# Kernel optimization log

Hardware: AMD Instinct MI355X
Metric: run time of the kernel (lower is better)

## Reference

```python
import jax, jax.numpy as jnp
import numpy as np

B, L, DIN, DOUT, H, N, NLAYERS, NRES, NSPECIES = 32, 2048, 5, 5, 256, 32, 4, 3, 100


def conv1d(x, w, b, pad):
    # x: (B, Cin, L), w: (Cout, Cin, K)
    y = jax.lax.conv_general_dilated(x, w, (1,), [(pad, pad)], dimension_numbers=('NCH', 'OIH', 'NCH'))
    return y + b[None, :, None]


def layer_norm_c(x, g, b):
    # LayerNorm over channel dim of (B, H, L) (matches norm(x.transpose(-1,-2)).transpose(-1,-2))
    mu = x.mean(1, keepdims=True)
    v = ((x - mu) ** 2).mean(1, keepdims=True)
    return (x - mu) / jnp.sqrt(v + 1e-5) * g[None, :, None] + b[None, :, None]


def dss_layer(x, log_dt, lam_re, lam_im, W_re, W_im, D, glu_w, glu_b):
    # Bidirectional diagonal state-space (DSS) layer, transposed layout (B, H, L).
    Bb, Hh, Ll = x.shape
    dt = jnp.exp(log_dt)                                  # (H,)
    lam = lam_re + 1j * lam_im                            # (N,) with Re(lam) < 0
    pos = jnp.arange(Ll)
    # Vandermonde: E[h,n,l] = exp(dt[h] * lam[n] * l)
    E = jnp.exp(dt[:, None, None] * lam[None, :, None] * pos[None, None, :])  # (H,N,L) complex
    W = W_re + 1j * W_im                                  # (2,H,N) fwd/bwd kernels
    k = jnp.einsum('chn,hnl->chl', W, E).real             # (2,H,L)
    zpad = jnp.zeros_like(k[0])
    k2 = jnp.concatenate([k[0], zpad], -1) + jnp.concatenate([zpad, k[1][:, ::-1]], -1)  # (H,2L)
    # FFT circular conv of length 2L -> linear conv, keep first L
    y = jnp.fft.irfft(jnp.fft.rfft(x, 2 * Ll) * jnp.fft.rfft(k2, 2 * Ll)[None], 2 * Ll)[..., :Ll]
    y = y + D[None, :, None] * x
    y = jax.nn.gelu(y, approximate=False)
    # postact GLU via position-wise linear H -> 2H
    z = jnp.einsum('oh,bhl->bol', glu_w, y) + glu_b[None, :, None]
    return z[:, :Hh] * jax.nn.sigmoid(z[:, Hh:])


def setup_inputs():
    key = jax.random.key(0)
    ks = jax.random.split(key, 20)
    g = lambda i, shape, s=0.05: jax.random.normal(ks[i], shape, jnp.float32) * s
    inp = {}
    inp['x'] = jax.random.normal(ks[0], (B, DIN, L), jnp.float32)
    inp['xs'] = jax.random.randint(ks[1], (B,), 0, NSPECIES)
    inp['enc_w'] = g(2, (H, DIN, 15))
    inp['enc_b'] = jnp.zeros((H,), jnp.float32)
    inp['res_w1'] = g(3, (NRES, H, H, 3), 0.02)
    inp['res_b1'] = jnp.zeros((NRES, H), jnp.float32)
    inp['res_w2'] = g(4, (NRES, H, H, 3), 0.02)
    inp['res_b2'] = jnp.zeros((NRES, H), jnp.float32)
    inp['log_dt'] = jax.random.uniform(ks[5], (NLAYERS, H), jnp.float32, float(np.log(1e-3)), float(np.log(1e-1)))
    inp['lam_re'] = -(0.1 + jax.random.uniform(ks[6], (NLAYERS, N), jnp.float32))
    inp['lam_im'] = jnp.broadcast_to(jnp.pi * jnp.arange(N, dtype=jnp.float32), (NLAYERS, N)) + 0.0
    inp['W_re'] = g(7, (NLAYERS, 2, H, N), 0.1)
    inp['W_im'] = g(8, (NLAYERS, 2, H, N), 0.1)
    inp['D'] = g(9, (NLAYERS, H), 1.0)
    inp['glu_w'] = g(10, (NLAYERS, 2 * H, H))
    inp['glu_b'] = jnp.zeros((NLAYERS, 2 * H), jnp.float32)
    inp['ln_g'] = jnp.ones((NLAYERS, H), jnp.float32)
    inp['ln_b'] = jnp.zeros((NLAYERS, H), jnp.float32)
    inp['dec_w'] = g(11, (DOUT, H, 15))
    inp['dec_b'] = jnp.zeros((DOUT,), jnp.float32)
    inp['sp_emb'] = g(12, (NSPECIES, H), 0.02)
    inp['h1_w'] = g(13, (128, 256)); inp['h1_b'] = jnp.zeros((128,), jnp.float32)
    inp['h2_w'] = g(14, (64, 128)); inp['h2_b'] = jnp.zeros((64,), jnp.float32)
    inp['h3_w'] = g(15, (32, 64)); inp['h3_b'] = jnp.zeros((32,), jnp.float32)
    inp['h4_w'] = g(16, (1, 32)); inp['h4_b'] = jnp.zeros((1,), jnp.float32)
    return inp


def _forward(x, xs, enc_w, enc_b, res_w1, res_b1, res_w2, res_b2, log_dt, lam_re, lam_im, W_re, W_im, D, glu_w, glu_b, ln_g, ln_b, dec_w, dec_b, sp_emb, h1_w, h1_b, h2_w, h2_b, h3_w, h3_b, h4_w, h4_b):
    h = conv1d(x, enc_w, enc_b, 7)
    for i in range(NRES):  # L1Block resnet stack (dropout/BN are identity at eval)
        r = jax.nn.relu(conv1d(h, res_w1[i], res_b1[i], 1))
        r = conv1d(r, res_w2[i], res_b2[i], 1)
        h = jax.nn.relu(r + h)
    for i in range(NLAYERS):  # post-norm DSS blocks
        z = dss_layer(h, log_dt[i], lam_re[i], lam_im[i], W_re[i], W_im[i], D[i], glu_w[i], glu_b[i])
        h = layer_norm_c(z + h, ln_g[i], ln_b[i])
    h = h + sp_emb[xs][:, :, None]  # species encoder (embed_before=False)
    seq_emb = h
    agg = h.mean(-1)  # (B, H)
    r = jax.nn.elu(agg @ h1_w.T + h1_b)
    r = jax.nn.elu(r @ h2_w.T + h2_b)
    r = jax.nn.elu(r @ h3_w.T + h3_b)
    reg_y = r @ h4_w.T + h4_b
    dec = conv1d(h, dec_w, dec_b, 7)
    return dec, seq_emb, reg_y


def reference(x, xs, enc_w, enc_b, res_w1, res_b1, res_w2, res_b2, log_dt, lam_re, lam_im, W_re, W_im, D, glu_w, glu_b, ln_g, ln_b, dec_w, dec_b, sp_emb, h1_w, h1_b, h2_w, h2_b, h3_w, h3_b, h4_w, h4_b):
    return _forward(x, xs, enc_w, enc_b, res_w1, res_b1, res_w2, res_b2, log_dt, lam_re, lam_im, W_re, W_im, D, glu_w, glu_b, ln_g, ln_b, dec_w, dec_b, sp_emb, h1_w, h1_b, h2_w, h2_b, h3_w, h3_b, h4_w, h4_b)
```

## Files before the change

kernel.cpp:

```cpp
#include <hip/hip_runtime.h>
#include <math.h>

#define B 32
#define L 2048
#define DIN 5
#define DOUT 5
#define H 256
#define NST 32
#define NLAYERS 4
#define NRES 3
#define CHUNK 128
#define NCH 16
#define LSEQ (B*H*L)

typedef __attribute__((ext_vector_type(8))) _Float16 half8;
typedef __attribute__((ext_vector_type(4))) float f32x4;

__device__ __forceinline__ float gelu_fast(float v) {
    float x = v * 0.7071067811865475f;
    float ax = fabsf(x);
    float t = 1.f / fmaf(0.3275911f, ax, 1.f);
    float poly = t*(0.254829592f + t*(-0.284496736f + t*(1.421413741f +
                 t*(-1.453152027f + t*1.061405429f))));
    float e = __expf(-ax*ax);
    float erfv = copysignf(1.f - poly*e, x);
    return 0.5f * v * (1.f + erfv);
}
#define SWZ(r) ((((r) ^ ((r) >> 2)) & 3))
#define LDIDX(l, c) ((l)*281 + ((c)>>5)*35 + ((c)&31))

__global__ void k_wenc(const float* __restrict__ ew, _Float16* __restrict__ wenc) {
    int idx = blockIdx.x*256 + threadIdx.x;
    if (idx >= 256*96) return;
    int o = idx / 96, kk = idx % 96;
    int ci = kk >> 4, k = kk & 15;
    float v = (ci < DIN && k < 15) ? ew[(o*DIN + ci)*15 + k] : 0.f;
    wenc[idx] = (_Float16)v;
}

__global__ __launch_bounds__(256) void k_enc(const float* __restrict__ x,
        const _Float16* __restrict__ wenc, const float* __restrict__ bias,
        _Float16* __restrict__ out) {
    __shared__ _Float16 a_lds[3*128*32];
    __shared__ _Float16 b_lds[3*128*32];
    const int tid = threadIdx.x;
    const int mbase = blockIdx.x * 128;
    const int oh = blockIdx.y;
    const int b = mbase >> 11;
    const int lbase = mbase & 2047;
    const int lane = tid & 63;
    const int w = tid >> 6;
    const int wm = (w >> 1) * 64, wn = (w & 1) * 64;
    const int fr = lane & 15, kg = lane >> 4;

    #pragma unroll
    for (int i = 0; i < 6; ++i) {
        int g = i*256 + tid;
        int r = g / 12, rem = g % 12;
        int ks = rem >> 2, q = rem & 3;
        int kk0 = ks*32 + q*8;
        int ci = kk0 >> 4, k0 = kk0 & 15;
        half8 va;
        #pragma unroll
        for (int e = 0; e < 8; ++e) {
            int k = k0 + e;
            int l = lbase + r - 7 + k;
            float v = (ci < DIN && k < 15 && l >= 0 && l < L)
                        ? x[((size_t)(b*DIN + ci))*L + l] : 0.f;
            va[e] = (_Float16)v;
        }
        *(half8*)&a_lds[ks*4096 + r*32 + ((q ^ SWZ(r))*8)] = va;
        uint4 vb = *(const uint4*)&wenc[(size_t)(oh*128 + r)*96 + kk0];
        *(uint4*)&b_lds[ks*4096 + r*32 + ((q ^ SWZ(r))*8)] = vb;
    }
    __syncthreads();
    f32x4 acc[4][4];
    #pragma unroll
    for (int i = 0; i < 4; ++i)
        #pragma unroll
        for (int j = 0; j < 4; ++j)
            #pragma unroll
            for (int k = 0; k < 4; ++k) acc[i][j][k] = 0.f;
    #pragma unroll
    for (int ks = 0; ks < 3; ++ks) {
        half8 af[4], bfr[4];
        #pragma unroll
        for (int mf = 0; mf < 4; ++mf) {
            int ra = wm + mf*16 + fr;
            af[mf] = *(const half8*)&a_lds[ks*4096 + ra*32 + ((kg ^ SWZ(ra))*8)];
        }
        #pragma unroll
        for (int nf = 0; nf < 4; ++nf) {
            int rb = wn + nf*16 + fr;
            bfr[nf] = *(const half8*)&b_lds[ks*4096 + rb*32 + ((kg ^ SWZ(rb))*8)];
        }
        #pragma unroll
        for (int mf = 0; mf < 4; ++mf)
            #pragma unroll
            for (int nf = 0; nf < 4; ++nf)
                acc[mf][nf] = __builtin_amdgcn_mfma_f32_16x16x32_f16(af[mf], bfr[nf], acc[mf][nf], 0, 0, 0);
    }
    #pragma unroll
    for (int nf = 0; nf < 4; ++nf) {
        int o = oh*128 + wn + nf*16 + fr;
        float bo = bias[o];
        #pragma unroll
        for (int mf = 0; mf < 4; ++mf)
            #pragma unroll
            for (int rg = 0; rg < 4; ++rg) {
                size_t m = (size_t)mbase + wm + mf*16 + kg*4 + rg;
                out[m*256 + o] = (_Float16)(acc[mf][nf][rg] + bo);
            }
    }
}

__global__ void k_wpack(const float* __restrict__ w1, const float* __restrict__ w2,
                        _Float16* __restrict__ wpk) {
    int idx = blockIdx.x*256 + threadIdx.x;
    if (idx >= NRES*2*3*65536) return;
    int ci = idx & 255;
    int o  = (idx >> 8) & 255;
    int k  = (idx >> 16) % 3;
    int cv = idx / (3*65536);
    const float* src = (cv & 1) ? w2 : w1;
    wpk[idx] = (_Float16)src[(((cv>>1)*H + o)*H + ci)*3 + k];
}

__global__ __launch_bounds__(256) void k_t_cf16(const _Float16* __restrict__ in,
        _Float16* __restrict__ out) {
    __shared__ float t[64][65];
    int tid = threadIdx.x;
    int l0 = blockIdx.x*64, c0 = blockIdx.y*64, b = blockIdx.z;
    #pragma unroll
    for (int i = 0; i < 2; ++i) {
        int g = i*256 + tid;
        int c8 = (g & 7) * 8, l = g >> 3;
        half8 v = *(const half8*)&in[((size_t)b*L + l0 + l)*256 + c0 + c8];
        #pragma unroll
        for (int e = 0; e < 8; ++e) t[c8 + e][l] = (float)v[e];
    }
    __syncthreads();
    #pragma unroll
    for (int i = 0; i < 2; ++i) {
        int g = i*256 + tid;
        int l8 = (g & 7) * 8, c = g >> 3;
        half8 hv;
        #pragma unroll
        for (int e = 0; e < 8; ++e) hv[e] = (_Float16)t[c][l8 + e];
        *(half8*)&out[((size_t)(b*H + c0 + c))*L + l0 + l8] = hv;
    }
}

__global__ __launch_bounds__(256) void k_t16(const _Float16* __restrict__ in,
                                             _Float16* __restrict__ out) {
    __shared__ float t[64][65];
    int tid = threadIdx.x;
    int l0 = blockIdx.x*64, c0 = blockIdx.y*64, b = blockIdx.z;
    #pragma unroll
    for (int i = 0; i < 2; ++i) {
        int g = i*256 + tid;
        int l8 = (g & 7) * 8, c = g >> 3;
        half8 v = *(const half8*)&in[((size_t)(b*H + c0 + c))*L + l0 + l8];
        #pragma unroll
        for (int e = 0; e < 8; ++e) t[c][l8 + e] = (float)v[e];
    }
    __syncthreads();
    #pragma unroll
    for (int i = 0; i < 2; ++i) {
        int g = i*256 + tid;
        int c8 = (g & 7) * 8, l = g >> 3;
        half8 hv;
        #pragma unroll
        for (int e = 0; e < 8; ++e) hv[e] = (_Float16)t[c8 + e][l];
        *(half8*)&out[((size_t)b*L + l0 + l)*256 + c0 + c8] = hv;
    }
}

template<bool RESID>
__global__ __launch_bounds__(256, 2) void k_cv3(const _Float16* __restrict__ xin,
        const _Float16* __restrict__ wpk, const float* __restrict__ bias,
        const _Float16* __restrict__ resid, _Float16* __restrict__ out) {
    __shared__ _Float16 a_lds[128*32];
    __shared__ _Float16 b_lds[256*32];
    __shared__ float    ep[32*256];
    const int tid = threadIdx.x;
    const int mbase = blockIdx.x * 128;
    const int lane = tid & 63;
    const int w = tid >> 6;
    const int wm = (w >> 1) * 64, wo = (w & 1) * 128;
    const int fr = lane & 15, kg = lane >> 4;

    const int r0s = tid >> 2, q0 = tid & 3;
    const int sq = SWZ(r0s);
    const int awA0 = r0s*32 + ((q0 ^ sq) * 8);
    const int awA1 = (64 + r0s)*32 + ((q0 ^ SWZ(64 + r0s)) * 8);

    f32x4 acc[4][8];
    #pragma unroll
    for (int i = 0; i < 4; ++i)
        #pragma unroll
        for (int j = 0; j < 8; ++j)
            #pragma unroll
            for (int k = 0; k < 4; ++k) acc[i][j][k] = 0.f;

    uint4 pa0, pa1, pb[4];
    auto loadstep = [&](int kk, uint4& a0, uint4& a1, uint4 (&bb)[4]) {
        const int koff = kk >> 3, cic = kk & 7;
        const int cb = cic*32 + q0*8;
        {
            int m = mbase + r0s;
            int ll = (m & (L-1)) + koff - 1;
            a0 = (ll >= 0 && ll < L) ? *(const uint4*)&xin[((size_t)(m + koff - 1))*256 + cb]
                                     : make_uint4(0,0,0,0);
            int m1 = mbase + 64 + r0s;
            int l1 = (m1 & (L-1)) + koff - 1;
            a1 = (l1 >= 0 && l1 < L) ? *(const uint4*)&xin[((size_t)(m1 + koff - 1))*256 + cb]
                                     : make_uint4(0,0,0,0);
        }
        #pragma unroll
        for (int u = 0; u < 4; ++u)
            bb[u] = *(const uint4*)&wpk[((size_t)(koff*256 + u*64 + r0s))*256 + cb];
    };
    loadstep(0, pa0, pa1, pb);
    for (int kk = 0; kk < 24; ++kk) {
        __syncthreads();
        *(uint4*)&a_lds[awA0] = pa0;
        *(uint4*)&a_lds[awA1] = pa1;
        #pragma unroll
        for (int u = 0; u < 4; ++u)
            *(uint4*)&b_lds[(u*64 + r0s)*32 + ((q0 ^ sq)*8)] = pb[u];
        uint4 na0 = make_uint4(0,0,0,0), na1 = na0, nb[4] = {na0, na0, na0, na0};
        if (kk < 23) loadstep(kk+1, na0, na1, nb);
        __syncthreads();
        half8 af[4];
        #pragma unroll
        for (int mf = 0; mf < 4; ++mf) {
            int ra = wm + mf*16 + fr;
            af[mf] = *(const half8*)&a_lds[ra*32 + ((kg ^ SWZ(ra)) * 8)];
        }
        #pragma unroll
        for (int nf = 0; nf < 8; ++nf) {
            int rb = wo + nf*16 + fr;
            half8 bfr = *(const half8*)&b_lds[rb*32 + ((kg ^ SWZ(rb)) * 8)];
            #pragma unroll
            for (int mf = 0; mf < 4; ++mf)
                acc[mf][nf] = __builtin_amdgcn_mfma_f32_16x16x32_f16(af[mf], bfr, acc[mf][nf], 0, 0, 0);
        }
        pa0 = na0; pa1 = na1;
        #pragma unroll
        for (int u = 0; u < 4; ++u) pb[u] = nb[u];
    }
    float bo8[8];
    #pragma unroll
    for (int nf = 0; nf < 8; ++nf) bo8[nf] = bias[wo + nf*16 + fr];
    const int er = tid >> 3, eoc = (tid & 7) * 32;
    #pragma unroll
    for (int mf = 0; mf < 4; ++mf) {
        __syncthreads();
        #pragma unroll
        for (int nf = 0; nf < 8; ++nf) {
            int o = wo + nf*16 + fr;
            int srb = (w >> 1)*16 + kg*4;
            #pragma unroll
            for (int rg = 0; rg < 4; ++rg)
                ep[(srb + rg)*256 + o] = acc[mf][nf][rg] + bo8[nf];
        }
        __syncthreads();
        size_t m = (size_t)mbase + mf*16 + (er < 16 ? er : 48 + er);
        #pragma unroll
        for (int u = 0; u < 4; ++u) {
            float4 v0 = *(float4*)&ep[er*256 + eoc + u*8];
            float4 v1 = *(float4*)&ep[er*256 + eoc + u*8 + 4];
            float vv[8] = {v0.x, v0.y, v0.z, v0.w, v1.x, v1.y, v1.z, v1.w};
            if (RESID) {
                half8 rv = *(const half8*)&resid[m*256 + eoc + u*8];
                #pragma unroll
                for (int e = 0; e < 8; ++e) vv[e] += (float)rv[e];
            }
            half8 hv;
            #pragma unroll
            for (int e = 0; e < 8; ++e) hv[e] = (_Float16)fmaxf(vv[e], 0.f);
            *(half8*)&out[m*256 + eoc + u*8] = hv;
        }
    }
}

__global__ __launch_bounds__(128) void k_wkern(const float* __restrict__ log_dt,
        const float* __restrict__ lam_re, const float* __restrict__ lam_im,
        const float* __restrict__ W_re, const float* __restrict__ W_im,
        const float* __restrict__ Dv, const float* __restrict__ gw,
        _Float16* __restrict__ wbigA, _Float16* __restrict__ wbigB,
        _Float16* __restrict__ wg_all,
        _Float16* __restrict__ zp_all, float4* __restrict__ zwb_all) {
    __shared__ float kf[128], kb[128];
    __shared__ _Float16 E16[128*130];
    const int hh = blockIdx.x;
    const int layer = blockIdx.y;
    const int t = threadIdx.x;
    float dt = expf(log_dt[layer*H + hh]);
    float skf = 0.f, skb = 0.f;
    for (int n = 0; n < 32; ++n) {
        float a  = dt * lam_re[layer*NST + n];
        float bi = dt * lam_im[layer*NST + n];
        float wfr = W_re[((layer*2+0)*H + hh)*NST + n];
        float wfi = W_im[((layer*2+0)*H + hh)*NST + n];
        float wbr = W_re[((layer*2+1)*H + hh)*NST + n];
        float wbi = W_im[((layer*2+1)*H + hh)*NST + n];
        float e0 = expf(a*t), s0, c0; sincosf(bi*t, &s0, &c0);
        float zr0 = e0*c0, zi0 = e0*s0;
        skf = fmaf(wfr, zr0, skf) - wfi*zi0;
        skb = fmaf(wbr, zr0, skb) - wbi*zi0;
        float e1 = expf(a*(t+1)), s1, c1; sincosf(bi*(t+1), &s1, &c1);
        float zr1 = e1*c1, zi1 = e1*s1;
        E16[t*130 + n]      = (_Float16)(wfr*zr1 - wfi*zi1);
        E16[t*130 + 32 + n] = (_Float16)(-(wfr*zi1 + wfi*zr1));
        float e2 = expf(a*(127-t)), s2, c2; sincosf(bi*(127-t), &s2, &c2);
        float zr2 = e2*c2, zi2 = e2*s2;
        E16[t*130 + 64 + n] = (_Float16)(wbr*zr2 - wbi*zi2);
        E16[t*130 + 96 + n] = (_Float16)(-(wbr*zi2 + wbi*zr2));
    }
    kf[t] = skf + ((t == 0) ? Dv[layer*H + hh] : 0.f);
    kb[t] = skb;
    __syncthreads();
    _Float16* dst = (layer < 2 ? wbigA + (size_t)layer*H*32768
                               : wbigB + (size_t)(layer-2)*H*32768)
                    + (size_t)hh*32768;
    for (int g = t; g < 4096; g += 128) {
        int tt = g >> 5;
        int k0 = (g & 31) * 8;
        half8 hv;
        if (k0 < 128) {
            #pragma unroll
            for (int e = 0; e < 8; ++e) {
                int k = k0 + e;
                hv[e] = (_Float16)((k <= tt) ? kf[tt - k] : kb[k - tt - 1]);
            }
        } else {
            #pragma unroll
            for (int e = 0; e < 8; ++e)
                hv[e] = E16[tt*130 + (k0 - 128) + e];
        }
        *(half8*)&dst[g*8] = hv;
    }
    const float* gsrc = &gw[(size_t)layer*131072 + (size_t)hh*512];
    _Float16* gdst = &wg_all[(size_t)layer*131072 + (size_t)hh*512];
    {
        int j8 = t * 4;
        float4 v = *(const float4*)&gsrc[j8];
        _Float16 h4[4] = {(_Float16)v.x, (_Float16)v.y, (_Float16)v.z, (_Float16)v.w};
        *(uint2*)&gdst[j8] = *(uint2*)h4;
    }
    {
        int dn = t >> 1, c = t & 1, dir = dn >> 5, n = dn & 31;
        float a  = dt * lam_re[layer*NST + n];
        float bi = dt * lam_im[layer*NST + n];
        float er = expf(a);
        float zre = er * cosf(bi), zim = er * sinf(bi);
        if (c == 0 && dir == 0) {
            float eC = expf(a * (float)CHUNK);
            float s, co; sincosf(bi * (float)CHUNK, &s, &co);
            zwb_all[layer*H*NST + hh*NST + n] = make_float4(zre, zim, eC*co, eC*s);
        }
        _Float16* zdst = &zp_all[(size_t)layer*H*16384 + (size_t)hh*16384 + t*128];
        float cr = 1.f, ci = 0.f;
        for (int p8 = 0; p8 < 128; p8 += 8) {
            half8 buf;
            #pragma unroll
            for (int e = 0; e < 8; ++e) {
                float val = c ? ci : cr;
                if (dir) buf[e] = (_Float16)val;
                else     buf[7 - e] = (_Float16)val;
                float nr = cr*zre - ci*zim;
                float ni = cr*zim + ci*zre;
                cr = nr; ci = ni;
            }
            if (dir) *(half8*)&zdst[p8] = buf;
            else     *(half8*)&zdst[120 - p8] = buf;
        }
    }
}

__global__ void k_wdec(const float* __restrict__ dw, _Float16* __restrict__ wdk) {
    int idx = blockIdx.x*256 + threadIdx.x;
    if (idx >= 15*16*256) return;
    int cfull = idx & 255;
    int o = (idx >> 8) & 15;
    int k = idx >> 12;
    float v = (o < DOUT) ? dw[(o*H + cfull)*15 + k] : 0.f;
    int cc = cfull >> 5, cl = cfull & 31;
    int cq = cl >> 3, cb = cl & 7;
    wdk[cc*7680 + (k*16 + o)*32 + ((cq ^ SWZ(o))*8) + cb] = (_Float16)v;
}

__global__ __launch_bounds__(256, 4) void k_dss(const _Float16* __restrict__ hm16,
        const _Float16* __restrict__ zp, const _Float16* __restrict__ wbig,
        const float4* __restrict__ zwb, _Float16* __restrict__ y16) {
    __shared__ _Float16 xbuf[4*32*32];
    __shared__ _Float16 bbuf[2*128*32];
    __shared__ float    sbuf[32*128];
    _Float16* sb16 = (_Float16*)sbuf;

    const int tid = threadIdx.x;
    const int hh = blockIdx.x;
    const int b0 = blockIdx.y * 2;
    const int lane = tid & 63;
    const int w = tid >> 6;
    const int wn = w * 32;
    const int fr = lane & 15, kg = lane >> 4;

    #pragma unroll
    for (int i = 0; i < 2; ++i) {
        int g = i*256 + tid;
        int m = g >> 4, gi = g & 15;
        int kc = gi >> 2, q = gi & 3;
        uint4 v = *(const uint4*)&hm16[((size_t)((b0 + (m>>4))*H + hh))*L
                                       + (m&15)*128 + kc*32 + q*8];
        *(uint4*)&xbuf[kc*1024 + m*32 + ((q ^ SWZ(m))*8)] = v;
    }

    f32x4 acc1[2][2];
    #pragma unroll
    for (int i = 0; i < 2; ++i)
        #pragma unroll
        for (int j = 0; j < 2; ++j)
            #pragma unroll
            for (int k = 0; k < 4; ++k) acc1[i][j][k] = 0.f;
    const _Float16* zb = &zp[(size_t)hh*16384];
    const int gr0 = tid >> 2, gq0 = tid & 3;
    const int gr1 = 64 + gr0;
    const int bw0 = gr0*32 + ((gq0 ^ SWZ(gr0))*8);
    const int bw1 = gr1*32 + ((gq0 ^ SWZ(gr1))*8);
    uint4 pb0 = *(const uint4*)&zb[gr0*128 + gq0*8];
    uint4 pb1 = *(const uint4*)&zb[gr1*128 + gq0*8];
    *(uint4*)&bbuf[bw0] = pb0;
    *(uint4*)&bbuf[bw1] = pb1;
    pb0 = *(const uint4*)&zb[gr0*128 + 32 + gq0*8];
    pb1 = *(const uint4*)&zb[gr1*128 + 32 + gq0*8];
    __syncthreads();
    for (int kc = 0; kc < 4; ++kc) {
        if (kc < 3) {
            *(uint4*)&bbuf[((kc+1)&1)*4096 + bw0] = pb0;
            *(uint4*)&bbuf[((kc+1)&1)*4096 + bw1] = pb1;
            if (kc < 2) {
                pb0 = *(const uint4*)&zb[gr0*128 + (kc+2)*32 + gq0*8];
                pb1 = *(const uint4*)&zb[gr1*128 + (kc+2)*32 + gq0*8];
            }
        }
        half8 af[2], bf2[2];
        #pragma unroll
        for (int mf = 0; mf < 2; ++mf) {
            int ra = mf*16 + fr;
            af[mf] = *(const half8*)&xbuf[kc*1024 + ra*32 + ((kg ^ SWZ(ra))*8)];
        }
        #pragma unroll
        for (int nf = 0; nf < 2; ++nf) {
            int rb = wn + nf*16 + fr;
            bf2[nf] = *(const half8*)&bbuf[(kc&1)*4096 + rb*32 + ((kg ^ SWZ(rb))*8)];
        }
        #pragma unroll
        for (int mf = 0; mf < 2; ++mf)
            #pragma unroll
            for (int nf = 0; nf < 2; ++nf)
                acc1[mf][nf] = __builtin_amdgcn_mfma_f32_16x16x32_f16(af[mf], bf2[nf], acc1[mf][nf], 0, 0, 0);
        __syncthreads();
    }
    #pragma unroll
    for (int mf = 0; mf < 2; ++mf)
        #pragma unroll
        for (int nf = 0; nf < 2; ++nf)
            #pragma unroll
            for (int rg = 0; rg < 4; ++rg)
                sbuf[(mf*16 + kg*4 + rg)*128 + wn + nf*16 + fr] = acc1[mf][nf][rg];
    __syncthreads();

    {
        int b_loc = tid >> 6, dn = tid & 63;
        if (b_loc < 2) {
            int dir = dn >> 5, n = dn & 31;
            float4 z4 = zwb[hh*NST + n];
            float zcre = z4.z, zcim = z4.w;
            int q1 = n >> 3, e1 = n & 7;
            float pre = 0.f, pim = 0.f;
            for (int s = 0; s < NCH; ++s) {
                int ch = dir ? (NCH - 1 - s) : s;
                int m = b_loc*16 + ch;
                bbuf[(dir*2 + 0)*1024 + m*32 + ((q1 ^ SWZ(m))*8) + e1] = (_Float16)pre;
                bbuf[(dir*2 + 1)*1024 + m*32 + ((q1 ^ SWZ(m))*8) + e1] = (_Float16)pim;
                float cre = sbuf[m*128 + dn*2];
                float cim = sbuf[m*128 + dn*2 + 1];
                float nre = fmaf(zcre, pre, fmaf(-zcim, pim, cre));
                float nim = fmaf(zcre, pim, fmaf(zcim, pre, cim));
                pre = nre; pim = nim;
            }
        }
    }
    __syncthreads();

    f32x4 acc3[2][2];
    #pragma unroll
    for (int i = 0; i < 2; ++i)
        #pragma unroll
        for (int j = 0; j < 2; ++j)
            #pragma unroll
            for (int k = 0; k < 4; ++k) acc3[i][j][k] = 0.f;
    const _Float16* wb = &wbig[(size_t)hh*32768];
    pb0 = *(const uint4*)&wb[gr0*256 + gq0*8];
    pb1 = *(const uint4*)&wb[gr1*256 + gq0*8];
    *(uint4*)&sb16[bw0] = pb0;
    *(uint4*)&sb16[bw1] = pb1;
    pb0 = *(const uint4*)&wb[gr0*256 + 32 + gq0*8];
    pb1 = *(const uint4*)&wb[gr1*256 + 32 + gq0*8];
    __syncthreads();
    for (int kc = 0; kc < 8; ++kc) {
        if (kc < 7) {
            *(uint4*)&sb16[((kc+1)&1)*4096 + bw0] = pb0;
            *(uint4*)&sb16[((kc+1)&1)*4096 + bw1] = pb1;
            if (kc < 6) {
                pb0 = *(const uint4*)&wb[gr0*256 + (kc+2)*32 + gq0*8];
                pb1 = *(const uint4*)&wb[gr1*256 + (kc+2)*32 + gq0*8];
            }
        }
        half8 af[2], bf2[2];
        #pragma unroll
        for (int mf = 0; mf < 2; ++mf) {
            int ra = mf*16 + fr;
            af[mf] = (kc < 4)
                ? *(const half8*)&xbuf[kc*1024 + ra*32 + ((kg ^ SWZ(ra))*8)]
                : *(const half8*)&bbuf[(kc-4)*1024 + ra*32 + ((kg ^ SWZ(ra))*8)];
        }
        #pragma unroll
        for (int nf = 0; nf < 2; ++nf) {
            int rb = wn + nf*16 + fr;
            bf2[nf] = *(const half8*)&sb16[(kc&1)*4096 + rb*32 + ((kg ^ SWZ(rb))*8)];
        }
        #pragma unroll
        for (int mf = 0; mf < 2; ++mf)
            #pragma unroll
            for (int nf = 0; nf < 2; ++nf)
                acc3[mf][nf] = __builtin_amdgcn_mfma_f32_16x16x32_f16(af[mf], bf2[nf], acc3[mf][nf], 0, 0, 0);
        __syncthreads();
    }
    _Float16* yst = sb16;
    #pragma unroll
    for (int mf = 0; mf < 2; ++mf) {
        #pragma unroll
        for (int rg = 0; rg < 4; ++rg) {
            int m = mf*16 + kg*4 + rg;
            #pragma unroll
            for (int nf = 0; nf < 2; ++nf) {
                int t = wn + nf*16 + fr;
                yst[m*136 + t] = (_Float16)gelu_fast(acc3[mf][nf][rg]);
            }
        }
    }
    __syncthreads();
    {
        int r = tid >> 3, tc = (tid & 7) * 16;
        size_t gb = ((size_t)((b0 + (r>>4))*H + hh))*L + (r&15)*128;
        *(half8*)&y16[gb + tc]     = *(half8*)&yst[r*136 + tc];
        *(half8*)&y16[gb + tc + 8] = *(half8*)&yst[r*136 + tc + 8];
    }
}

__global__ __launch_bounds__(256) void k_glu16(const _Float16* __restrict__ yt,
        const _Float16* __restrict__ wg, const float* __restrict__ bias,
        _Float16* __restrict__ zc) {
    __shared__ _Float16 a_lds[128*32];
    __shared__ _Float16 b_lds[128*32];
    __shared__ float    ep[32*64];
    const int tid = threadIdx.x;
    const int mbase = blockIdx.x * 128;
    const int o0 = blockIdx.y * 64;
    const int lane = tid & 63;
    const int w = tid >> 6;
    const int wm = (w >> 1) * 64, wn = (w & 1) * 32;
    const int fr = lane & 15, kg = lane >> 4;
    const int r0s = tid >> 2, q0 = tid & 3;
    const int r1s = 64 + r0s;
    const int aw0 = r0s*32 + ((q0 ^ SWZ(r0s)) * 8);
    const int aw1 = r1s*32 + ((q0 ^ SWZ(r1s)) * 8);
    const int og0 = o0 + r0s;
    const int og1 = 256 + o0 + r0s;

    f32x4 accg[4][2], accs[4][2];
    #pragma unroll
    for (int i = 0; i < 4; ++i)
        #pragma unroll
        for (int j = 0; j < 2; ++j)
            #pragma unroll
            for (int k = 0; k < 4; ++k) { accg[i][j][k] = 0.f; accs[i][j][k] = 0.f; }

    uint4 pa0, pa1, pb0, pb1;
    auto loadstep = [&](int kc, uint4& a0, uint4& a1, uint4& b0, uint4& b1) {
        const int cb = kc*32 + q0*8;
        a0 = *(const uint4*)&yt[((size_t)(mbase + r0s))*256 + cb];
        a1 = *(const uint4*)&yt[((size_t)(mbase + r1s))*256 + cb];
        b0 = *(const uint4*)&wg[((size_t)og0)*256 + cb];
        b1 = *(const uint4*)&wg[((size_t)og1)*256 + cb];
    };
    loadstep(0, pa0, pa1, pb0, pb1);
    for (int kc = 0; kc < 8; ++kc) {
        __syncthreads();
        *(uint4*)&a_lds[aw0] = pa0;
        *(uint4*)&a_lds[aw1] = pa1;
        *(uint4*)&b_lds[aw0] = pb0;
        *(uint4*)&b_lds[aw1] = pb1;
        uint4 na0 = make_uint4(0,0,0,0), na1 = na0, nb0 = na0, nb1 = na0;
        if (kc < 7) loadstep(kc+1, na0, na1, nb0, nb1);
        __syncthreads();
        half8 af[4], bg[2], bs[2];
        #pragma unroll
        for (int mf = 0; mf < 4; ++mf) {
            int ra = wm + mf*16 + fr;
            af[mf] = *(const half8*)&a_lds[ra*32 + ((kg ^ SWZ(ra)) * 8)];
        }
        #pragma unroll
        for (int nf = 0; nf < 2; ++nf) {
            int rb = wn + nf*16 + fr;
            bg[nf] = *(const half8*)&b_lds[rb*32 + ((kg ^ SWZ(rb)) * 8)];
            int rb2 = 64 + rb;
            bs[nf] = *(const half8*)&b_lds[rb2*32 + ((kg ^ SWZ(rb2)) * 8)];
        }
        #pragma unroll
        for (int mf = 0; mf < 4; ++mf)
            #pragma unroll
            for (int nf = 0; nf < 2; ++nf) {
                accg[mf][nf] = __builtin_amdgcn_mfma_f32_16x16x32_f16(af[mf], bg[nf], accg[mf][nf], 0, 0, 0);
                accs[mf][nf] = __builtin_amdgcn_mfma_f32_16x16x32_f16(af[mf], bs[nf], accs[mf][nf], 0, 0, 0);
            }
        pa0 = na0; pa1 = na1; pb0 = nb0; pb1 = nb1;
    }
    float b0v[2], b1v[2];
    #pragma unroll
    for (int nf = 0; nf < 2; ++nf) {
        int o = o0 + wn + nf*16 + fr;
        b0v[nf] = bias[o]; b1v[nf] = bias[256 + o];
    }
    const int er = tid >> 3, eoc = (tid & 7) * 8;
    #pragma unroll
    for (int mf = 0; mf < 4; ++mf) {
        __syncthreads();
        #pragma unroll
        for (int nf = 0; nf < 2; ++nf) {
            int ol = wn + nf*16 + fr;
            int srb = (w >> 1)*16 + kg*4;
            #pragma unroll
            for (int rg = 0; rg < 4; ++rg) {
                float g = accg[mf][nf][rg] + b0v[nf];
                float s = accs[mf][nf][rg] + b1v[nf];
                ep[(srb + rg)*64 + ol] = g / (1.f + expf(-s));
            }
        }
        __syncthreads();
        size_t m = (size_t)mbase + mf*16 + (er < 16 ? er : 48 + er);
        float4 v0 = *(float4*)&ep[er*64 + eoc];
        float4 v1 = *(float4*)&ep[er*64 + eoc + 4];
        half8 hv;
        hv[0]=(_Float16)v0.x; hv[1]=(_Float16)v0.y; hv[2]=(_Float16)v0.z; hv[3]=(_Float16)v0.w;
        hv[4]=(_Float16)v1.x; hv[5]=(_Float16)v1.y; hv[6]=(_Float16)v1.z; hv[7]=(_Float16)v1.w;
        *(half8*)&zc[m*256 + o0 + eoc] = hv;
    }
}

template<bool SP>
__global__ __launch_bounds__(256) void k_ln2(const _Float16* __restrict__ zc,
        _Float16* __restrict__ hm, const float* __restrict__ g, const float* __restrict__ bb,
        const int* __restrict__ xs, const float* __restrict__ emb,
        float* __restrict__ outseq) {
    __shared__ float tl[8992];
    int tid = threadIdx.x;
    int b = blockIdx.y;
    int l0 = blockIdx.x * 32;
    for (int j = tid; j < 1024; j += 256) {
        int c = j >> 2, l8 = (j & 3) * 8;
        half8 v = *(const half8*)&hm[((size_t)(b*H + c))*L + l0 + l8];
        #pragma unroll
        for (int e = 0; e < 8; ++e) tl[LDIDX(l8 + e, c)] = (float)v[e];
    }
    __syncthreads();
    int r = tid >> 3, p = tid & 7;
    float v[32];
    float sum = 0.f, ss = 0.f;
    const _Float16* zrow = &zc[((size_t)(b*L + l0 + r))*256 + p*32];
    #pragma unroll
    for (int q = 0; q < 4; ++q) {
        half8 z8 = *(const half8*)&zrow[q*8];
        #pragma unroll
        for (int i = 0; i < 8; ++i) {
            float hv = tl[LDIDX(r, p*32 + q*8 + i)];
            float vv = (float)z8[i] + hv;
            v[q*8+i] = vv;
            sum += vv; ss = fmaf(vv, vv, ss);
        }
    }
    sum += __shfl_xor(sum, 1); ss += __shfl_xor(ss, 1);
    sum += __shfl_xor(sum, 2); ss += __shfl_xor(ss, 2);
    sum += __shfl_xor(sum, 4); ss += __shfl_xor(ss, 4);
    float mu = sum * (1.f/256.f);
    float var = ss * (1.f/256.f) - mu*mu;
    float rs = rsqrtf(var + 1e-5f);
    int sp = SP ? xs[b] : 0;
    #pragma unroll
    for (int q = 0; q < 32; ++q) {
        int c = p*32 + q;
        float val = (v[q] - mu) * rs * g[c] + bb[c];
        if (SP) val += emb[sp*H + c];
        tl[LDIDX(r, c)] = val;
    }
    __syncthreads();
    for (int j = tid; j < 1024; j += 256) {
        int c = j >> 2, l8 = (j & 3) * 8;
        float fv[8];
        half8 hv;
        #pragma unroll
        for (int e = 0; e < 8; ++e) {
            fv[e] = tl[LDIDX(l8 + e, c)];
            hv[e] = (_Float16)fv[e];
        }
        *(half8*)&hm[((size_t)(b*H + c))*L + l0 + l8] = hv;
        if (SP) {
            *(float4*)&outseq[((size_t)(b*H + c))*L + l0 + l8] = make_float4(fv[0],fv[1],fv[2],fv[3]);
            *(float4*)&outseq[((size_t)(b*H + c))*L + l0 + l8 + 4] = make_float4(fv[4],fv[5],fv[6],fv[7]);
        }
    }
}

__global__ __launch_bounds__(128) void k_dec(const _Float16* __restrict__ ht,
        const _Float16* __restrict__ wdk, const float* __restrict__ bias,
        float* __restrict__ outdec) {
    __shared__ _Float16 a_lds[160*32];
    __shared__ _Float16 b_lds[15*16*32];
    const int tid = threadIdx.x;
    const int mbase = blockIdx.x * 128;
    const int b = mbase >> 11;
    const int lbase = mbase & 2047;
    const int lane = tid & 63;
    const int w = tid >> 6;
    const int fr = lane & 15, kg = lane >> 4;
    const int rs = tid >> 2, q0 = tid & 3;
    f32x4 acc[4];
    #pragma unroll
    for (int i = 0; i < 4; ++i)
        #pragma unroll
        for (int k = 0; k < 4; ++k) acc[i][k] = 0.f;
    for (int cc = 0; cc < 8; ++cc) {
        __syncthreads();
        #pragma unroll
        for (int ps = 0; ps < 5; ++ps) {
            int r = ps*32 + rs;
            if (r < 142) {
                int l = lbase - 7 + r;
                uint4 v = (l >= 0 && l < L) ? *(const uint4*)&ht[((size_t)(b*L + l))*256 + cc*32 + q0*8]
                                            : make_uint4(0,0,0,0);
                *(uint4*)&a_lds[r*32 + ((q0 ^ SWZ(r))*8)] = v;
            }
        }
        for (int jj = tid; jj < 960; jj += 128)
            *(uint4*)&b_lds[jj*8] = *(const uint4*)&wdk[cc*7680 + jj*8];
        __syncthreads();
        #pragma unroll
        for (int k = 0; k < 15; ++k) {
            half8 bfr = *(const half8*)&b_lds[(k*16 + fr)*32 + ((kg ^ SWZ(fr))*8)];
            #pragma unroll
            for (int mf = 0; mf < 4; ++mf) {
                int ra = w*64 + mf*16 + fr + k;
                half8 af = *(const half8*)&a_lds[ra*32 + ((kg ^ SWZ(ra))*8)];
                acc[mf] = __builtin_amdgcn_mfma_f32_16x16x32_f16(af, bfr, acc[mf], 0, 0, 0);
            }
        }
    }
    if (fr < DOUT) {
        float bo = bias[fr];
        #pragma unroll
        for (int mf = 0; mf < 4; ++mf)
            #pragma unroll
            for (int rg = 0; rg < 4; ++rg) {
                int m = mbase + w*64 + mf*16 + kg*4 + rg;
                outdec[((size_t)(b*DOUT + fr))*L + (m & 2047)] = acc[mf][rg] + bo;
            }
    }
}

__global__ __launch_bounds__(256) void k_agg(const _Float16* __restrict__ h, float* __restrict__ agg) {
    __shared__ float red[256];
    int bc = blockIdx.x;
    int tid = threadIdx.x;
    half8 v = *(const half8*)&h[(size_t)bc*L + tid*8];
    float s = 0.f;
    #pragma unroll
    for (int e = 0; e < 8; ++e) s += (float)v[e];
    red[tid] = s; __syncthreads();
    for (int k = 128; k > 0; k >>= 1) {
        if (tid < k) red[tid] += red[tid+k];
        __syncthreads();
    }
    if (tid == 0) agg[bc] = red[0] * (1.f/(float)L);
}

__global__ __launch_bounds__(128) void k_mlp(const float* __restrict__ agg,
        const float* __restrict__ w1, const float* __restrict__ b1,
        const float* __restrict__ w2, const float* __restrict__ b2,
        const float* __restrict__ w3, const float* __restrict__ b3,
        const float* __restrict__ w4, const float* __restrict__ b4,
        float* __restrict__ outreg) {
    __shared__ float a0[256], r1[128], r2[64], r3[32];
    int b = blockIdx.x, tid = threadIdx.x;
    a0[tid] = agg[b*256 + tid];
    a0[tid+128] = agg[b*256 + tid + 128];
    __syncthreads();
    {
        float s = b1[tid];
        for (int k = 0; k < 256; ++k) s = fmaf(w1[tid*256+k], a0[k], s);
        r1[tid] = s > 0.f ? s : expm1f(s);
    }
    __syncthreads();
    if (tid < 64) {
        float s = b2[tid];
        for (int k = 0; k < 128; ++k) s = fmaf(w2[tid*128+k], r1[k], s);
        r2[tid] = s > 0.f ? s : expm1f(s);
    }
    __syncthreads();
    if (tid < 32) {
        float s = b3[tid];
        for (int k = 0; k < 64; ++k) s = fmaf(w3[tid*64+k], r2[k], s);
        r3[tid] = s > 0.f ? s : expm1f(s);
    }
    __syncthreads();
    if (tid == 0) {
        float s = b4[0];
        for (int k = 0; k < 32; ++k) s = fmaf(w4[k], r3[k], s);
        outreg[b] = s;
    }
}

extern "C" void kernel_launch(void* const* d_in, const int* in_sizes, int n_in,
                              void* d_out, int out_size, void* d_ws, size_t ws_size,
                              hipStream_t stream) {
    const float* x      = (const float*)d_in[0];
    const int*   xs     = (const int*)d_in[1];
    const float* enc_w  = (const float*)d_in[2];
    const float* enc_b  = (const float*)d_in[3];
    const float* res_w1 = (const float*)d_in[4];
    const float* res_b1 = (const float*)d_in[5];
    const float* res_w2 = (const float*)d_in[6];
    const float* res_b2 = (const float*)d_in[7];
    const float* log_dt = (const float*)d_in[8];
    const float* lam_re = (const float*)d_in[9];
    const float* lam_im = (const float*)d_in[10];
    const float* W_re   = (const float*)d_in[11];
    const float* W_im   = (const float*)d_in[12];
    const float* Dv     = (const float*)d_in[13];
    const float* glu_w  = (const float*)d_in[14];
    const float* glu_b  = (const float*)d_in[15];
    const float* ln_g   = (const float*)d_in[16];
    const float* ln_b   = (const float*)d_in[17];
    const float* dec_w  = (const float*)d_in[18];
    const float* dec_b  = (const float*)d_in[19];
    const float* sp_emb = (const float*)d_in[20];
    const float* h1_w = (const float*)d_in[21]; const float* h1_b = (const float*)d_in[22];
    const float* h2_w = (const float*)d_in[23]; const float* h2_b = (const float*)d_in[24];
    const float* h3_w = (const float*)d_in[25]; const float* h3_b = (const float*)d_in[26];
    const float* h4_w = (const float*)d_in[27]; const float* h4_b = (const float*)d_in[28];

    float* ws   = (float*)d_ws;
    _Float16* hm16 = (_Float16*)ws;
    _Float16* zp_all = (_Float16*)(ws + (size_t)LSEQ/2);
    float* t1   = ws + (size_t)LSEQ;
    float* t2   = ws + (size_t)2*LSEQ;
    _Float16* xb  = (_Float16*)t1;
    _Float16* xa  = (_Float16*)t1 + (size_t)LSEQ;
    _Float16* wpk = (_Float16*)t2;
    _Float16* yt     = (_Float16*)t1;
    _Float16* wbigA  = (_Float16*)t1 + (size_t)LSEQ;
    _Float16* y16    = (_Float16*)t2;
    _Float16* zc16   = (_Float16*)t2;
    _Float16* wbigB  = (_Float16*)t2 + (size_t)LSEQ;
    _Float16* dect   = (_Float16*)t1;
    float* tail = ws + (size_t)3*LSEQ;
    _Float16* wg_all = (_Float16*)tail;
    float4* zwb_all  = (float4*)(tail + 262144);
    float* aggb = tail + 262144 + 131072;
    _Float16* wdk = (_Float16*)(aggb + 8192);
    _Float16* wenc = wdk + 61440;

    float* outdec = (float*)d_out;
    float* outseq = outdec + B*DOUT*L;
    float* outreg = outseq + (size_t)LSEQ;

    k_wenc<<<96, 256, 0, stream>>>(enc_w, wenc);
    k_enc<<<dim3(B*L/128, 2), 256, 0, stream>>>(x, wenc, enc_b, xa);

    k_wpack<<<(NRES*2*3*65536 + 255)/256, 256, 0, stream>>>(res_w1, res_w2, wpk);
    for (int r = 0; r < NRES; ++r) {
        k_cv3<false><<<B*L/128, 256, 0, stream>>>(
            xa, wpk + (size_t)(r*2+0)*3*65536, res_b1 + r*H, nullptr, xb);
        k_cv3<true><<<B*L/128, 256, 0, stream>>>(
            xb, wpk + (size_t)(r*2+1)*3*65536, res_b2 + r*H, xa, xa);
    }
    k_t_cf16<<<dim3(L/64, H/64, B), 256, 0, stream>>>(xa, hm16);

    k_wkern<<<dim3(H, NLAYERS), 128, 0, stream>>>(log_dt, lam_re, lam_im, W_re, W_im,
                                                  Dv, glu_w, wbigA, wbigB, wg_all,
                                                  zp_all, zwb_all);

    for (int i = 0; i < NLAYERS; ++i) {
        _Float16* wbig_i = (i < 2) ? (wbigA + (size_t)i*H*32768)
                                   : (wbigB + (size_t)(i-2)*H*32768);
        k_dss<<<dim3(H, 16), 256, 0, stream>>>(hm16,
                zp_all + (size_t)i*H*16384, wbig_i,
                zwb_all + (size_t)i*H*NST, y16);
        k_t16<<<dim3(L/64, H/64, B), 256, 0, stream>>>(y16, yt);
        k_glu16<<<dim3(B*L/128, 4), 256, 0, stream>>>(yt, wg_all + (size_t)i*131072,
                                                      glu_b + i*512, zc16);
        if (i < NLAYERS - 1)
            k_ln2<false><<<dim3(L/32, B), 256, 0, stream>>>(zc16, hm16, ln_g + i*H, ln_b + i*H,
                                                            nullptr, nullptr, nullptr);
        else
            k_ln2<true><<<dim3(L/32, B), 256, 0, stream>>>(zc16, hm16, ln_g + i*H, ln_b + i*H,
                                                           xs, sp_emb, outseq);
    }

    k_agg<<<B*H, 256, 0, stream>>>(hm16, aggb);
    k_mlp<<<B, 128, 0, stream>>>(aggb, h1_w, h1_b, h2_w, h2_b, h3_w, h3_b, h4_w, h4_b, outreg);
    k_t16<<<dim3(L/64, H/64, B), 256, 0, stream>>>(hm16, dect);
    k_wdec<<<(15*16*256 + 255)/256, 256, 0, stream>>>(dec_w, wdk);
    k_dec<<<B*L/128, 128, 0, stream>>>(dect, wdk, dec_b, outdec);
}
```

Baseline: 936.7 us.

## Double-buffer LDS in conv3 GEMM and derive Vandermonde terms by complex multiplication

The k=3 conv GEMM kernel now ping-pongs two LDS buffers, aliasing the epilogue scratch onto them, so each K-step needs one barrier instead of two and global loads run two steps ahead. The kernel-generation kernel replaces two of its three exp/sincos evaluations per state with complex multiplications by precomputed z^1 and z^127 powers. The double buffering raises register pressure from the prefetch depth. The division by |z^t|^2 can lose accuracy or overflow for strongly decaying modes.

```diff
diff --git a/kernel.cpp b/kernel.cpp
--- a/kernel.cpp
+++ b/kernel.cpp
@@ -180,9 +180,10 @@
 __global__ __launch_bounds__(256, 2) void k_cv3(const _Float16* __restrict__ xin,
         const _Float16* __restrict__ wpk, const float* __restrict__ bias,
         const _Float16* __restrict__ resid, _Float16* __restrict__ out) {
-    __shared__ _Float16 a_lds[128*32];
-    __shared__ _Float16 b_lds[256*32];
-    __shared__ float    ep[32*256];
+    __shared__ _Float16 smem[24576];
+    _Float16* a_lds = smem;
+    _Float16* b_lds = smem + 8192;
+    float* ep = (float*)smem;
     const int tid = threadIdx.x;
     const int mbase = blockIdx.x * 128;
     const int lane = tid & 63;
@@ -194,6 +195,7 @@
     const int sq = SWZ(r0s);
     const int awA0 = r0s*32 + ((q0 ^ sq) * 8);
     const int awA1 = (64 + r0s)*32 + ((q0 ^ SWZ(64 + r0s)) * 8);
+    const int bwr = r0s*32 + ((q0 ^ sq) * 8);
 
     f32x4 acc[4][8];
     #pragma unroll
@@ -222,33 +224,41 @@
             bb[u] = *(const uint4*)&wpk[((size_t)(koff*256 + u*64 + r0s))*256 + cb];
     };
     loadstep(0, pa0, pa1, pb);
+    *(uint4*)&a_lds[awA0] = pa0;
+    *(uint4*)&a_lds[awA1] = pa1;
+    #pragma unroll
+    for (int u = 0; u < 4; ++u)
+        *(uint4*)&b_lds[u*64*32 + bwr] = pb[u];
+    loadstep(1, pa0, pa1, pb);
+    __syncthreads();
     for (int kk = 0; kk < 24; ++kk) {
-        __syncthreads();
-        *(uint4*)&a_lds[awA0] = pa0;
-        *(uint4*)&a_lds[awA1] = pa1;
-        #pragma unroll
-        for (int u = 0; u < 4; ++u)
-            *(uint4*)&b_lds[(u*64 + r0s)*32 + ((q0 ^ sq)*8)] = pb[u];
-        uint4 na0 = make_uint4(0,0,0,0), na1 = na0, nb[4] = {na0, na0, na0, na0};
-        if (kk < 23) loadstep(kk+1, na0, na1, nb);
-        __syncthreads();
+        const int rsA = (kk & 1) * 4096;
+        const int rsB = (kk & 1) * 8192;
+        if (kk < 23) {
+            const int wsA = ((kk+1) & 1) * 4096;
+            const int wsB = ((kk+1) & 1) * 8192;
+            *(uint4*)&a_lds[wsA + awA0] = pa0;
+            *(uint4*)&a_lds[wsA + awA1] = pa1;
+            #pragma unroll
+            for (int u = 0; u < 4; ++u)
+                *(uint4*)&b_lds[wsB + u*64*32 + bwr] = pb[u];
+            if (kk < 22) loadstep(kk+2, pa0, pa1, pb);
+        }
         half8 af[4];
         #pragma unroll
         for (int mf = 0; mf < 4; ++mf) {
             int ra = wm + mf*16 + fr;
-            af[mf] = *(const half8*)&a_lds[ra*32 + ((kg ^ SWZ(ra)) * 8)];
+            af[mf] = *(const half8*)&a_lds[rsA + ra*32 + ((kg ^ SWZ(ra)) * 8)];
         }
         #pragma unroll
         for (int nf = 0; nf < 8; ++nf) {
             int rb = wo + nf*16 + fr;
-            half8 bfr = *(const half8*)&b_lds[rb*32 + ((kg ^ SWZ(rb)) * 8)];
+            half8 bfr = *(const half8*)&b_lds[rsB + rb*32 + ((kg ^ SWZ(rb)) * 8)];
             #pragma unroll
             for (int mf = 0; mf < 4; ++mf)
                 acc[mf][nf] = __builtin_amdgcn_mfma_f32_16x16x32_f16(af[mf], bfr, acc[mf][nf], 0, 0, 0);
         }
-        pa0 = na0; pa1 = na1;
-        #pragma unroll
-        for (int u = 0; u < 4; ++u) pb[u] = nb[u];
+        __syncthreads();
     }
     float bo8[8];
     #pragma unroll
@@ -294,10 +304,22 @@
         _Float16* __restrict__ zp_all, float4* __restrict__ zwb_all) {
     __shared__ float kf[128], kb[128];
     __shared__ _Float16 E16[128*130];
+    __shared__ float zn_lds[64], z127_lds[64];
     const int hh = blockIdx.x;
     const int layer = blockIdx.y;
     const int t = threadIdx.x;
     float dt = expf(log_dt[layer*H + hh]);
+    if (t < 32) {
+        float a  = dt * lam_re[layer*NST + t];
+        float bi = dt * lam_im[layer*NST + t];
+        float er = expf(a), s, c;
+        sincosf(bi, &s, &c);
+        zn_lds[2*t] = er*c;  zn_lds[2*t+1] = er*s;
+        float e7 = expf(127.f*a), s7, c7;
+        sincosf(127.f*bi, &s7, &c7);
+        z127_lds[2*t] = e7*c7;  z127_lds[2*t+1] = e7*s7;
+    }
+    __syncthreads();
     float skf = 0.f, skb = 0.f;
     for (int n = 0; n < 32; ++n) {
         float a  = dt * lam_re[layer*NST + n];
@@ -310,12 +332,15 @@
         float zr0 = e0*c0, zi0 = e0*s0;
         skf = fmaf(wfr, zr0, skf) - wfi*zi0;
         skb = fmaf(wbr, zr0, skb) - wbi*zi0;
-        float e1 = expf(a*(t+1)), s1, c1; sincosf(bi*(t+1), &s1, &c1);
-        float zr1 = e1*c1, zi1 = e1*s1;
+        float znr = zn_lds[2*n], zni = zn_lds[2*n+1];
+        float zr1 = zr0*znr - zi0*zni;
+        float zi1 = zr0*zni + zi0*znr;
         E16[t*130 + n]      = (_Float16)(wfr*zr1 - wfi*zi1);
         E16[t*130 + 32 + n] = (_Float16)(-(wfr*zi1 + wfi*zr1));
-        float e2 = expf(a*(127-t)), s2, c2; sincosf(bi*(127-t), &s2, &c2);
-        float zr2 = e2*c2, zi2 = e2*s2;
+        float inv = 1.f / (e0*e0);
+        float z7r = z127_lds[2*n], z7i = z127_lds[2*n+1];
+        float zr2 = (z7r*zr0 + z7i*zi0) * inv;
+        float zi2 = (z7i*zr0 - z7r*zi0) * inv;
         E16[t*130 + 64 + n] = (_Float16)(wbr*zr2 - wbi*zi2);
         E16[t*130 + 96 + n] = (_Float16)(-(wbr*zi2 + wbi*zr2));
     }
```

Result: slower. 1.104 ms (+17.9%).
